# Kernel tuning notes

Hardware: AMD Instinct MI355X
Metric: run time of the kernel (lower is better)

## Reference

```python
import jax, jax.numpy as jnp
import numpy as np

EMBED = 1024
HEADS = 16
HEAD_DIM = EMBED // HEADS


def setup_inputs() -> dict:
    key = jax.random.key(0)
    ks = jax.random.split(key, 8)
    B, S = 2, 2048
    inp = {
        "values": jax.random.normal(ks[0], (B, S, EMBED), jnp.float32),
        "keys": jax.random.normal(ks[1], (B, S, EMBED), jnp.float32),
        "queries": jax.random.normal(ks[2], (B, S, EMBED), jnp.float32),
        # per-head projection weights (torch Linear: y = x @ W.T), shared across heads
        "Wv": jax.random.normal(ks[3], (HEAD_DIM, HEAD_DIM), jnp.float32) / np.sqrt(HEAD_DIM),
        "Wk": jax.random.normal(ks[4], (HEAD_DIM, HEAD_DIM), jnp.float32) / np.sqrt(HEAD_DIM),
        "Wq": jax.random.normal(ks[5], (HEAD_DIM, HEAD_DIM), jnp.float32) / np.sqrt(HEAD_DIM),
        "Wo": jax.random.normal(ks[6], (EMBED, EMBED), jnp.float32) / np.sqrt(EMBED),
        "bo": jax.random.normal(ks[7], (EMBED,), jnp.float32) * 0.02,
    }
    return inp


def reference(values, keys, queries, Wv, Wk, Wq, Wo, bo):
    B, S, _ = queries.shape
    # split heads: (B, H, S, D)
    def split(x):
        return x.reshape(B, -1, HEADS, HEAD_DIM).transpose(0, 2, 1, 3)
    v, k, q = split(values), split(keys), split(queries)
    # per-head linear projections (no bias): x @ W.T
    v = jnp.einsum('bhsd,ed->bhse', v, Wv)
    k = jnp.einsum('bhsd,ed->bhse', k, Wk)
    q = jnp.einsum('bhsd,ed->bhse', q, Wq)
    # scaled dot-product attention (naive, full matrix)
    scores = jnp.einsum('bhqd,bhkd->bhqk', q, k) / jnp.sqrt(jnp.float32(HEAD_DIM))
    attn = jax.nn.softmax(scores, axis=-1)
    out = jnp.einsum('bhqk,bhkd->bhqd', attn, v)
    # merge heads and output projection
    out = out.transpose(0, 2, 1, 3).reshape(B, S, EMBED)
    return out @ Wo.T + bo
```

## Files before the change

kernel.cpp:

```cpp
#include <hip/hip_runtime.h>
#include <stdint.h>

#define HEADS 16
#define HD    64
#define SEQ   2048
#define BATCH 2
#define EMB   1024

using short8  = __attribute__((ext_vector_type(8))) short;
using float4v = __attribute__((ext_vector_type(4))) float;
using f32x16  = __attribute__((ext_vector_type(16))) float;

__device__ __forceinline__ unsigned int f2bfr(float f) {
    return (__float_as_uint(f) + 0x8000u) >> 16;
}

__device__ __forceinline__ unsigned int cvt_pk_bf16(float lo, float hi) {
    unsigned int r;
    asm("v_cvt_pk_bf16_f32 %0, %1, %2" : "=v"(r) : "v"(lo), "v"(hi));
    return r;
}

__device__ __forceinline__ unsigned int dpp_xor1(unsigned int x) {
    return (unsigned int)__builtin_amdgcn_update_dpp(0, (int)x, 0xB1, 0xF, 0xF, true);
}

__device__ __forceinline__ short8 mk8(unsigned int a, unsigned int b,
                                      unsigned int c, unsigned int d) {
    union { unsigned int u[4]; short8 s; } x;
    x.u[0] = a; x.u[1] = b; x.u[2] = c; x.u[3] = d;
    return x.s;
}

__global__ __launch_bounds__(256) void proj_kernel(
    const float* __restrict__ Vx, const float* __restrict__ Kx, const float* __restrict__ Qx,
    const float* __restrict__ Wv, const float* __restrict__ Wk, const float* __restrict__ Wq,
    const float* __restrict__ Wo,
    unsigned short* __restrict__ Qp, unsigned short* __restrict__ Kp,
    unsigned short* __restrict__ Vt, unsigned short* __restrict__ Wob) {
    __shared__ __align__(16) unsigned short Ws[64 * 72];
    __shared__ __align__(16) unsigned short xs[64 * 72];
    __shared__ __align__(16) unsigned short vt2[64 * 72];

    const int t = threadIdx.x, w = t >> 6, lane = t & 63, cl = lane & 15, quad = lane >> 4;
    const int z  = blockIdx.z;

    if (z == 3) {
        int cb = blockIdx.y * 32 + blockIdx.x;
        int i = (cb * 256 + t) * 4;
        float4 v = *(const float4*)(Wo + i);
        uint2 o;
        o.x = f2bfr(v.x) | (f2bfr(v.y) << 16);
        o.y = f2bfr(v.z) | (f2bfr(v.w) << 16);
        *(uint2*)(Wob + i) = o;
        return;
    }

    const int bh = blockIdx.y;
    const int b  = bh >> 4, h = bh & 15;
    const int s0 = blockIdx.x * 64;

    const float* x = (z == 0) ? Qx : (z == 1) ? Kx : Vx;
    const float* W = (z == 0) ? Wq : (z == 1) ? Wk : Wv;
    const float scale = (z == 0) ? 0.18033688011112044f : 1.0f;

#pragma unroll
    for (int rep = 0; rep < 4; ++rep) {
        int idx = rep * 1024 + t * 4;
        int e = idx >> 6, d0 = idx & 63;
        float4 w4 = *(const float4*)(W + idx);
        uint2 pk;
        pk.x = f2bfr(w4.x * scale) | (f2bfr(w4.y * scale) << 16);
        pk.y = f2bfr(w4.z * scale) | (f2bfr(w4.w * scale) << 16);
        *(uint2*)(&Ws[e * 72 + d0]) = pk;

        int s = e;
        float4 v4 = *(const float4*)(x + (size_t)(b * SEQ + s0 + s) * EMB + h * 64 + d0);
        uint2 px;
        px.x = f2bfr(v4.x) | (f2bfr(v4.y) << 16);
        px.y = f2bfr(v4.z) | (f2bfr(v4.w) << 16);
        *(uint2*)(&xs[s * 72 + d0]) = px;
    }
    __syncthreads();

    short8 a0 = *(const short8*)(&xs[(w * 16 + cl) * 72 + quad * 8]);
    short8 a1 = *(const short8*)(&xs[(w * 16 + cl) * 72 + 32 + quad * 8]);
    float4v c[4];
#pragma unroll
    for (int nt = 0; nt < 4; ++nt) c[nt] = (float4v){0.f, 0.f, 0.f, 0.f};
#pragma unroll
    for (int nt = 0; nt < 4; ++nt) {
        short8 b0 = *(const short8*)(&Ws[(nt * 16 + cl) * 72 + quad * 8]);
        c[nt] = __builtin_amdgcn_mfma_f32_16x16x32_bf16(a0, b0, c[nt], 0, 0, 0);
        short8 b1 = *(const short8*)(&Ws[(nt * 16 + cl) * 72 + 32 + quad * 8]);
        c[nt] = __builtin_amdgcn_mfma_f32_16x16x32_bf16(a1, b1, c[nt], 0, 0, 0);
    }

    if (z < 2) {
        const int even = ((lane & 1) == 0);
        const unsigned int psel = even ? 0x03020706u : 0x07060302u;
        const int evoff = even ? 0 : 16;
        unsigned int* Pw = (unsigned int*)xs;
#pragma unroll
        for (int r = 0; r < 4; ++r) {
            unsigned int rr[4], wd[4];
#pragma unroll
            for (int nt = 0; nt < 4; ++nt)
                rr[nt] = __float_as_uint(c[nt][r]) + 0x8000u;
#pragma unroll
            for (int nt = 0; nt < 4; ++nt) {
                unsigned int nb = dpp_xor1(rr[nt]);
                wd[nt] = __builtin_amdgcn_perm(rr[nt], nb, psel);
            }
            int dwbase = (w * 16 + quad * 4 + r) * 36 + evoff + (cl >> 1);
            Pw[dwbase]     = even ? wd[0] : wd[2];
            Pw[dwbase + 8] = even ? wd[1] : wd[3];
        }
        unsigned short* outp = (z == 0) ? Qp : Kp;
        int sl = w * 16 + (lane >> 2), c0 = (lane & 3) * 16;
        uint4 o0 = *(const uint4*)(&xs[sl * 72 + c0]);
        uint4 o1 = *(const uint4*)(&xs[sl * 72 + c0 + 8]);
        size_t base = ((size_t)bh * SEQ + s0 + sl) * 64 + c0;
        *(uint4*)(outp + base)     = o0;
        *(uint4*)(outp + base + 8) = o1;
    } else {
#pragma unroll
        for (int nt = 0; nt < 4; ++nt) {
            uint2 pk;
            pk.x = f2bfr(c[nt][0]) | (f2bfr(c[nt][1]) << 16);
            pk.y = f2bfr(c[nt][2]) | (f2bfr(c[nt][3]) << 16);
            *(uint2*)(&vt2[(nt * 16 + cl) * 72 + w * 16 + quad * 4]) = pk;
        }
        __syncthreads();
        int e = t >> 2, sc0 = (t & 3) * 16;
        uint4 o0 = *(const uint4*)(&vt2[e * 72 + sc0]);
        uint4 o1 = *(const uint4*)(&vt2[e * 72 + sc0 + 8]);
        size_t base = ((size_t)bh * 64 + e) * SEQ + s0 + sc0;
        *(uint4*)(Vt + base)     = o0;
        *(uint4*)(Vt + base + 8) = o1;
    }
}

__global__ __launch_bounds__(256) void attn_kernel(
    const unsigned short* __restrict__ Qp, const unsigned short* __restrict__ Kp,
    const unsigned short* __restrict__ Vt, unsigned short* __restrict__ AO) {
    __shared__ __align__(16) unsigned short Ks[2][64 * 72];
    __shared__ __align__(16) unsigned short Vs[2][64 * 72];

    const int t = threadIdx.x;
    const int w = t >> 6, lane = t & 63;
    const int l31 = lane & 31, h = lane >> 5;

    const int lid = blockIdx.x;
    const int bh  = ((lid & 7) << 2) | ((lid >> 3) & 3);
    const int q0  = (lid >> 5) * 128;

    const size_t hbase = (size_t)bh * SEQ * 64;
    const unsigned short* Kbase = Kp + hbase;
    const unsigned short* Vbase = Vt + hbase;

    short8 qf[4];
    {
        const unsigned short* qr = Qp + hbase + (size_t)(q0 + w * 32 + l31) * 64 + h * 8;
#pragma unroll
        for (int dt = 0; dt < 4; ++dt) qf[dt] = *(const short8*)(qr + dt * 16);
    }

    short8 ones;
#pragma unroll
    for (int i = 0; i < 8; ++i) ones[i] = (short)0x3F80;

    f32x16 o0, o1, ls;
#pragma unroll
    for (int r = 0; r < 16; ++r) { o0[r] = 0.f; o1[r] = 0.f; ls[r] = 0.f; }

    const int srow = t >> 3;
    const int scol = (t & 7) * 8;

    uint4 kreg[2], vreg[2];
#pragma unroll
    for (int p = 0; p < 2; ++p) {
        int row = srow + p * 32;
        kreg[p] = *(const uint4*)(Kbase + row * 64 + scol);
        vreg[p] = *(const uint4*)(Vbase + (size_t)row * SEQ + scol);
    }

    for (int kc = 0; kc < SEQ / 64; ++kc) {
        const int buf = kc & 1;
#pragma unroll
        for (int p = 0; p < 2; ++p) {
            int row = srow + p * 32;
            *(uint4*)(&Ks[buf][row * 72 + scol]) = kreg[p];
            *(uint4*)(&Vs[buf][row * 72 + scol]) = vreg[p];
        }
        __syncthreads();
        if (kc + 1 < SEQ / 64) {
#pragma unroll
            for (int p = 0; p < 2; ++p) {
                int row = srow + p * 32;
                kreg[p] = *(const uint4*)(Kbase + (size_t)(kc + 1) * 4096 + row * 64 + scol);
                vreg[p] = *(const uint4*)(Vbase + (size_t)row * SEQ + (kc + 1) * 64 + scol);
            }
        }

        f32x16 s0, s1;
#pragma unroll
        for (int r = 0; r < 16; ++r) { s0[r] = 0.f; s1[r] = 0.f; }

        __builtin_amdgcn_s_setprio(1);
#pragma unroll
        for (int dt = 0; dt < 4; ++dt) {
            short8 k0 = *(const short8*)(&Ks[buf][l31 * 72 + dt * 16 + h * 8]);
            short8 k1 = *(const short8*)(&Ks[buf][(32 + l31) * 72 + dt * 16 + h * 8]);
            s0 = __builtin_amdgcn_mfma_f32_32x32x16_bf16(k0, qf[dt], s0, 0, 0, 0);
            s1 = __builtin_amdgcn_mfma_f32_32x32x16_bf16(k1, qf[dt], s1, 0, 0, 0);
        }
        __builtin_amdgcn_s_setprio(0);

#pragma unroll
        for (int r = 0; r < 16; ++r) {
            s0[r] = __builtin_amdgcn_exp2f(s0[r]);
            s1[r] = __builtin_amdgcn_exp2f(s1[r]);
        }

        short8 fr[4];
        {
            unsigned e0 = cvt_pk_bf16(s0[0],  s0[1]),  e1 = cvt_pk_bf16(s0[2],  s0[3]);
            unsigned e2 = cvt_pk_bf16(s0[4],  s0[5]),  e3 = cvt_pk_bf16(s0[6],  s0[7]);
            unsigned e4 = cvt_pk_bf16(s0[8],  s0[9]),  e5 = cvt_pk_bf16(s0[10], s0[11]);
            unsigned e6 = cvt_pk_bf16(s0[12], s0[13]), e7 = cvt_pk_bf16(s0[14], s0[15]);
            unsigned x0 = __shfl_xor(e0, 32), x1 = __shfl_xor(e1, 32);
            unsigned x2 = __shfl_xor(e2, 32), x3 = __shfl_xor(e3, 32);
            unsigned x4 = __shfl_xor(e4, 32), x5 = __shfl_xor(e5, 32);
            unsigned x6 = __shfl_xor(e6, 32), x7 = __shfl_xor(e7, 32);
            fr[0] = mk8(h ? x2 : e0, h ? x3 : e1, h ? e2 : x0, h ? e3 : x1);
            fr[1] = mk8(h ? x6 : e4, h ? x7 : e5, h ? e6 : x4, h ? e7 : x5);
        }
        {
            unsigned e0 = cvt_pk_bf16(s1[0],  s1[1]),  e1 = cvt_pk_bf16(s1[2],  s1[3]);
            unsigned e2 = cvt_pk_bf16(s1[4],  s1[5]),  e3 = cvt_pk_bf16(s1[6],  s1[7]);
            unsigned e4 = cvt_pk_bf16(s1[8],  s1[9]),  e5 = cvt_pk_bf16(s1[10], s1[11]);
            unsigned e6 = cvt_pk_bf16(s1[12], s1[13]), e7 = cvt_pk_bf16(s1[14], s1[15]);
            unsigned x0 = __shfl_xor(e0, 32), x1 = __shfl_xor(e1, 32);
            unsigned x2 = __shfl_xor(e2, 32), x3 = __shfl_xor(e3, 32);
            unsigned x4 = __shfl_xor(e4, 32), x5 = __shfl_xor(e5, 32);
            unsigned x6 = __shfl_xor(e6, 32), x7 = __shfl_xor(e7, 32);
            fr[2] = mk8(h ? x2 : e0, h ? x3 : e1, h ? e2 : x0, h ? e3 : x1);
            fr[3] = mk8(h ? x6 : e4, h ? x7 : e5, h ? e6 : x4, h ? e7 : x5);
        }

        __builtin_amdgcn_s_setprio(1);
#pragma unroll
        for (int c = 0; c < 4; ++c) {
            short8 bv0 = *(const short8*)(&Vs[buf][l31 * 72 + c * 16 + h * 8]);
            short8 bv1 = *(const short8*)(&Vs[buf][(32 + l31) * 72 + c * 16 + h * 8]);
            o0 = __builtin_amdgcn_mfma_f32_32x32x16_bf16(fr[c], bv0, o0, 0, 0, 0);
            o1 = __builtin_amdgcn_mfma_f32_32x32x16_bf16(fr[c], bv1, o1, 0, 0, 0);
            ls = __builtin_amdgcn_mfma_f32_32x32x16_bf16(fr[c], ones,  ls, 0, 0, 0);
        }
        __builtin_amdgcn_s_setprio(0);
    }

    float inv[16];
#pragma unroll
    for (int r = 0; r < 16; ++r) inv[r] = 1.0f / ls[r];
#pragma unroll
    for (int r = 0; r < 16; ++r) {
        int row = q0 + w * 32 + (r & 3) + 8 * (r >> 2) + 4 * h;
        size_t rb = hbase + (size_t)row * 64 + l31;
        AO[rb]      = (unsigned short)f2bfr(o0[r] * inv[r]);
        AO[rb + 32] = (unsigned short)f2bfr(o1[r] * inv[r]);
    }
}

__global__ __launch_bounds__(256) void outproj_kernel(
    const unsigned short* __restrict__ AO, const unsigned short* __restrict__ Wob,
    const float* __restrict__ bo, float* __restrict__ out) {
    const int t = threadIdx.x, w = t >> 6, lane = t & 63;
    const int l31 = lane & 31, h = lane >> 5;

    const int wid = blockIdx.x * 4 + w;
    const int mt  = wid >> 4;
    const int et  = wid & 15;
    const int m0  = mt * 32, e0 = et * 64;
    const int b   = m0 >> 11;
    const int s   = (m0 & 2047) + l31;

    const unsigned short* pA  = AO + ((size_t)(b * 16) * SEQ + s) * 64 + h * 8;
    const unsigned short* pB0 = Wob + (size_t)(e0 + l31) * EMB + h * 8;
    const unsigned short* pB1 = Wob + (size_t)(e0 + 32 + l31) * EMB + h * 8;

    f32x16 c0, c1;
#pragma unroll
    for (int r = 0; r < 16; ++r) { c0[r] = 0.f; c1[r] = 0.f; }

    short8 a_c[4], b0_c[4], b1_c[4];
#pragma unroll
    for (int k4 = 0; k4 < 4; ++k4) {
        a_c[k4]  = *(const short8*)(pA + k4 * 16);
        b0_c[k4] = *(const short8*)(pB0 + k4 * 16);
        b1_c[k4] = *(const short8*)(pB1 + k4 * 16);
    }

#pragma unroll
    for (int hh = 0; hh < 16; ++hh) {
        short8 a_n[4], b0_n[4], b1_n[4];
        if (hh + 1 < 16) {
            const unsigned short* pAn = pA + (size_t)(hh + 1) * SEQ * 64;
#pragma unroll
            for (int k4 = 0; k4 < 4; ++k4) {
                a_n[k4]  = *(const short8*)(pAn + k4 * 16);
                b0_n[k4] = *(const short8*)(pB0 + (hh + 1) * 64 + k4 * 16);
                b1_n[k4] = *(const short8*)(pB1 + (hh + 1) * 64 + k4 * 16);
            }
        }
#pragma unroll
        for (int k4 = 0; k4 < 4; ++k4) {
            c0 = __builtin_amdgcn_mfma_f32_32x32x16_bf16(a_c[k4], b0_c[k4], c0, 0, 0, 0);
            c1 = __builtin_amdgcn_mfma_f32_32x32x16_bf16(a_c[k4], b1_c[k4], c1, 0, 0, 0);
        }
        if (hh + 1 < 16) {
#pragma unroll
            for (int k4 = 0; k4 < 4; ++k4) {
                a_c[k4] = a_n[k4]; b0_c[k4] = b0_n[k4]; b1_c[k4] = b1_n[k4];
            }
        }
    }

    const float bias0 = bo[e0 + l31];
    const float bias1 = bo[e0 + 32 + l31];
#pragma unroll
    for (int r = 0; r < 16; ++r) {
        int m = m0 + (r & 3) + 8 * (r >> 2) + 4 * h;
        out[(size_t)m * EMB + e0 + l31]      = c0[r] + bias0;
        out[(size_t)m * EMB + e0 + 32 + l31] = c1[r] + bias1;
    }
}

extern "C" void kernel_launch(void* const* d_in, const int* in_sizes, int n_in,
                              void* d_out, int out_size, void* d_ws, size_t ws_size,
                              hipStream_t stream) {
    const float* values  = (const float*)d_in[0];
    const float* keys    = (const float*)d_in[1];
    const float* queries = (const float*)d_in[2];
    const float* Wv = (const float*)d_in[3];
    const float* Wk = (const float*)d_in[4];
    const float* Wq = (const float*)d_in[5];
    const float* Wo = (const float*)d_in[6];
    const float* bo = (const float*)d_in[7];
    float* out = (float*)d_out;

    char* ws = (char*)d_ws;
    unsigned short* Qp  = (unsigned short*)(ws);
    unsigned short* Kp  = (unsigned short*)(ws + (8u  << 20));
    unsigned short* Vt  = (unsigned short*)(ws + (16u << 20));
    unsigned short* AO  = (unsigned short*)(ws + (24u << 20));
    unsigned short* Wob = (unsigned short*)(ws + (32u << 20));

    proj_kernel<<<dim3(SEQ / 64, BATCH * HEADS, 4), dim3(256), 0, stream>>>(
        values, keys, queries, Wv, Wk, Wq, Wo, Qp, Kp, Vt, Wob);
    attn_kernel<<<dim3((SEQ / 128) * BATCH * HEADS), dim3(256), 0, stream>>>(Qp, Kp, Vt, AO);
    outproj_kernel<<<dim3((EMB / 64) * ((BATCH * SEQ) / 32) / 4), dim3(256), 0, stream>>>(
        AO, Wob, bo, out);
}
```

Before: 229.2 us.

## Split attention over two key halves and add a combine kernel

The attention kernel now splits each query tile's key range into two halves, doubling the grid. Each half writes unnormalized fp32 partial outputs and row sums, and a new combine kernel adds them, normalizes, and packs to bf16 for the output projection. The row-sum MFMA against a ones vector is replaced by a per-lane fp32 accumulation plus one cross-half shuffle, which removes a third of the PV MFMAs. The aim is better CU occupancy with more blocks, at the cost of an extra launch and roughly 32MB of fp32 partial traffic to write and read back.

```diff
diff --git a/kernel.cpp b/kernel.cpp
--- a/kernel.cpp
+++ b/kernel.cpp
@@ -143,7 +143,8 @@
 
 __global__ __launch_bounds__(256) void attn_kernel(
     const unsigned short* __restrict__ Qp, const unsigned short* __restrict__ Kp,
-    const unsigned short* __restrict__ Vt, unsigned short* __restrict__ AO) {
+    const unsigned short* __restrict__ Vt, float* __restrict__ AOf,
+    float* __restrict__ Lf) {
     __shared__ __align__(16) unsigned short Ks[2][64 * 72];
     __shared__ __align__(16) unsigned short Vs[2][64 * 72];
 
@@ -151,13 +152,18 @@
     const int w = t >> 6, lane = t & 63;
     const int l31 = lane & 31, h = lane >> 5;
 
-    const int lid = blockIdx.x;
-    const int bh  = ((lid & 7) << 2) | ((lid >> 3) & 3);
-    const int q0  = (lid >> 5) * 128;
+    const int lid  = blockIdx.x;
+    const int bh   = ((lid & 7) << 2) | ((lid >> 3) & 3);
+    const int rest = lid >> 5;
+    const int kh   = rest & 1;
+    const int kb   = kh * (SEQ / 2);
+    const int q0   = (rest >> 1) * 128;
 
     const size_t hbase = (size_t)bh * SEQ * 64;
     const unsigned short* Kbase = Kp + hbase;
     const unsigned short* Vbase = Vt + hbase;
+    float* AOh = AOf + (size_t)kh * ((size_t)BATCH * HEADS * SEQ * 64);
+    float* Lfh = Lf + kh * (BATCH * HEADS * SEQ);
 
     short8 qf[4];
     {
@@ -166,13 +172,10 @@
         for (int dt = 0; dt < 4; ++dt) qf[dt] = *(const short8*)(qr + dt * 16);
     }
 
-    short8 ones;
-#pragma unroll
-    for (int i = 0; i < 8; ++i) ones[i] = (short)0x3F80;
-
-    f32x16 o0, o1, ls;
-#pragma unroll
-    for (int r = 0; r < 16; ++r) { o0[r] = 0.f; o1[r] = 0.f; ls[r] = 0.f; }
+    f32x16 o0, o1;
+#pragma unroll
+    for (int r = 0; r < 16; ++r) { o0[r] = 0.f; o1[r] = 0.f; }
+    float lsum = 0.f;
 
     const int srow = t >> 3;
     const int scol = (t & 7) * 8;
@@ -181,11 +184,12 @@
 #pragma unroll
     for (int p = 0; p < 2; ++p) {
         int row = srow + p * 32;
-        kreg[p] = *(const uint4*)(Kbase + row * 64 + scol);
-        vreg[p] = *(const uint4*)(Vbase + (size_t)row * SEQ + scol);
-    }
-
-    for (int kc = 0; kc < SEQ / 64; ++kc) {
+        kreg[p] = *(const uint4*)(Kbase + (size_t)(kb + row) * 64 + scol);
+        vreg[p] = *(const uint4*)(Vbase + (size_t)row * SEQ + kb + scol);
+    }
+
+    const int NKC = SEQ / 128;
+    for (int kc = 0; kc < NKC; ++kc) {
         const int buf = kc & 1;
 #pragma unroll
         for (int p = 0; p < 2; ++p) {
@@ -194,12 +198,12 @@
             *(uint4*)(&Vs[buf][row * 72 + scol]) = vreg[p];
         }
         __syncthreads();
-        if (kc + 1 < SEQ / 64) {
+        if (kc + 1 < NKC) {
 #pragma unroll
             for (int p = 0; p < 2; ++p) {
                 int row = srow + p * 32;
-                kreg[p] = *(const uint4*)(Kbase + (size_t)(kc + 1) * 4096 + row * 64 + scol);
-                vreg[p] = *(const uint4*)(Vbase + (size_t)row * SEQ + (kc + 1) * 64 + scol);
+                kreg[p] = *(const uint4*)(Kbase + (size_t)(kb + (kc + 1) * 64 + row) * 64 + scol);
+                vreg[p] = *(const uint4*)(Vbase + (size_t)row * SEQ + kb + (kc + 1) * 64 + scol);
             }
         }
 
@@ -221,6 +225,13 @@
         for (int r = 0; r < 16; ++r) {
             s0[r] = __builtin_amdgcn_exp2f(s0[r]);
             s1[r] = __builtin_amdgcn_exp2f(s1[r]);
+        }
+
+        {
+            float ts = 0.f;
+#pragma unroll
+            for (int r = 0; r < 16; ++r) ts += s0[r] + s1[r];
+            lsum += ts;
         }
 
         short8 fr[4];
@@ -256,21 +267,36 @@
             short8 bv1 = *(const short8*)(&Vs[buf][(32 + l31) * 72 + c * 16 + h * 8]);
             o0 = __builtin_amdgcn_mfma_f32_32x32x16_bf16(fr[c], bv0, o0, 0, 0, 0);
             o1 = __builtin_amdgcn_mfma_f32_32x32x16_bf16(fr[c], bv1, o1, 0, 0, 0);
-            ls = __builtin_amdgcn_mfma_f32_32x32x16_bf16(fr[c], ones,  ls, 0, 0, 0);
         }
         __builtin_amdgcn_s_setprio(0);
     }
 
-    float inv[16];
-#pragma unroll
-    for (int r = 0; r < 16; ++r) inv[r] = 1.0f / ls[r];
 #pragma unroll
     for (int r = 0; r < 16; ++r) {
         int row = q0 + w * 32 + (r & 3) + 8 * (r >> 2) + 4 * h;
         size_t rb = hbase + (size_t)row * 64 + l31;
-        AO[rb]      = (unsigned short)f2bfr(o0[r] * inv[r]);
-        AO[rb + 32] = (unsigned short)f2bfr(o1[r] * inv[r]);
-    }
+        AOh[rb]      = o0[r];
+        AOh[rb + 32] = o1[r];
+    }
+    lsum += __shfl_xor(lsum, 32);
+    if (lane < 32) Lfh[bh * SEQ + q0 + w * 32 + lane] = lsum;
+}
+
+__global__ __launch_bounds__(256) void combine_kernel(
+    const float* __restrict__ AOf0, const float* __restrict__ AOf1,
+    const float* __restrict__ Lf0, const float* __restrict__ Lf1,
+    unsigned short* __restrict__ AO) {
+    size_t i = ((size_t)blockIdx.x * 256 + threadIdx.x) * 8;
+    int row = (int)(i >> 6);
+    float linv = 1.0f / (Lf0[row] + Lf1[row]);
+    float4 u0 = *(const float4*)(AOf0 + i), u1 = *(const float4*)(AOf0 + i + 4);
+    float4 v0 = *(const float4*)(AOf1 + i), v1 = *(const float4*)(AOf1 + i + 4);
+    uint4 o;
+    o.x = f2bfr((u0.x + v0.x) * linv) | (f2bfr((u0.y + v0.y) * linv) << 16);
+    o.y = f2bfr((u0.z + v0.z) * linv) | (f2bfr((u0.w + v0.w) * linv) << 16);
+    o.z = f2bfr((u1.x + v1.x) * linv) | (f2bfr((u1.y + v1.y) * linv) << 16);
+    o.w = f2bfr((u1.z + v1.z) * linv) | (f2bfr((u1.w + v1.w) * linv) << 16);
+    *(uint4*)(AO + i) = o;
 }
 
 __global__ __launch_bounds__(256) void outproj_kernel(
@@ -354,12 +380,20 @@
     unsigned short* Qp  = (unsigned short*)(ws);
     unsigned short* Kp  = (unsigned short*)(ws + (8u  << 20));
     unsigned short* Vt  = (unsigned short*)(ws + (16u << 20));
-    unsigned short* AO  = (unsigned short*)(ws + (24u << 20));
-    unsigned short* Wob = (unsigned short*)(ws + (32u << 20));
+    unsigned short* Wob = (unsigned short*)(ws + (24u << 20));
+    float*          AOf = (float*)(ws + (26u << 20));
+    float*          Lf  = (float*)(ws + (58u << 20));
+    unsigned short* AO  = Qp;
+
+    const size_t AOFH = (size_t)BATCH * HEADS * SEQ * 64;
+    const int    LFH  = BATCH * HEADS * SEQ;
 
     proj_kernel<<<dim3(SEQ / 64, BATCH * HEADS, 4), dim3(256), 0, stream>>>(
         values, keys, queries, Wv, Wk, Wq, Wo, Qp, Kp, Vt, Wob);
-    attn_kernel<<<dim3((SEQ / 128) * BATCH * HEADS), dim3(256), 0, stream>>>(Qp, Kp, Vt, AO);
+    attn_kernel<<<dim3((SEQ / 128) * BATCH * HEADS * 2), dim3(256), 0, stream>>>(
+        Qp, Kp, Vt, AOf, Lf);
+    combine_kernel<<<dim3((unsigned)(AOFH / (256 * 8))), dim3(256), 0, stream>>>(
+        AOf, AOf + AOFH, Lf, Lf + LFH, AO);
     outproj_kernel<<<dim3((EMB / 64) * ((BATCH * SEQ) / 32) / 4), dim3(256), 0, stream>>>(
         AO, Wob, bo, out);
 }
```

Result: slower. 241.8 us (+5.5%).
